# Kernel tuning notes

Hardware: AMD Instinct MI355X
Metric: run time of the kernel (lower is better)

Reference implementation:

```python
import jax, jax.numpy as jnp
import numpy as np

N, D, E, DFF = 8192, 1024, 8, 4096


def setup_inputs() -> dict:
    key = jax.random.key(0)
    k1, k2, k3, k4 = jax.random.split(key, 4)
    x = jax.random.normal(k1, (N, D), dtype=jnp.float32)
    gate_w = jax.random.normal(k2, (D, E), dtype=jnp.float32) * 0.02
    w1 = jax.random.normal(k3, (E, D, DFF), dtype=jnp.float32) * 0.02
    w2 = jax.random.normal(k4, (E, DFF, D), dtype=jnp.float32) * 0.02
    return {"x": x, "gate_w": gate_w, "w1": w1, "w2": w2, "top_k": 2}


def reference(x, gate_w, w1, w2, top_k):
    # Router: softmax over experts, top-k, renormalize top-k weights.
    gate_logits = x @ gate_w                          # [N, E]
    gate_probs = jax.nn.softmax(gate_logits, axis=-1)  # [N, E]
    top_w, top_i = jax.lax.top_k(gate_probs, top_k)    # [N, k]
    top_w = top_w / jnp.sum(top_w, axis=-1, keepdims=True)
    # Dense combine weights: zero except at the top-k experts per token.
    n = x.shape[0]
    dense_w = jnp.zeros_like(gate_probs).at[jnp.arange(n)[:, None], top_i].set(top_w)  # [N, E]
    # Per-expert SiLU MLP, weighted combine. Loop over small fixed E.
    y = jnp.zeros_like(x)
    for e in range(w1.shape[0]):
        h = jax.nn.silu(x @ w1[e]) @ w2[e]            # [N, D]
        y = y + dense_w[:, e:e + 1] * h
    return y
```

## Files before the change

### kernel.cpp

```cpp
#include <hip/hip_runtime.h>


#define N_TOK 8192
#define DIM   1024
#define NE    8
#define DFF   4096
#define BM 128
#define BN 128
#define BK 64
#define QE 4
#define KS2 2
#define NT2 (DFF / KS2 / BK)

typedef unsigned short u16;
typedef short bf16x8 __attribute__((ext_vector_type(8)));
typedef float f32x4  __attribute__((ext_vector_type(4)));

#define TOKE_OFF   0u
#define TOKW_OFF   32768u
#define TLIST_OFF  65536u
#define WLIST_OFF  131072u
#define COUNTS_OFF 196608u
#define BASEP_OFF  196672u
#define CURSOR_OFF 196736u
#define XB_OFF     1048576u
#define H_OFF      17825792u
#define WT_OFF     152043520u

__device__ __forceinline__ float bf2f(u16 h) {
    return __uint_as_float(((unsigned)h) << 16);
}
__device__ __forceinline__ u16 f2bf(float f) {
    unsigned u = __float_as_uint(f);
    unsigned r = u + 0x7FFFu + ((u >> 16) & 1u);
    return (u16)(r >> 16);
}

#define GLL16(g, l)                                                             \
    __builtin_amdgcn_global_load_lds(                                           \
        (const __attribute__((address_space(1))) unsigned int*)(g),             \
        (__attribute__((address_space(3))) unsigned int*)(l), 16, 0, 0)

__global__ __launch_bounds__(256) void convtrans(
        const float* __restrict__ in, u16* __restrict__ out, int R, int C) {
    __shared__ float t[32][33];
    int z = blockIdx.z;
    const float* src = in  + (size_t)z * R * C;
    u16*         dst = out + (size_t)z * R * C;
    int c0 = blockIdx.x * 32, r0 = blockIdx.y * 32;
    int tx = threadIdx.x & 7, ty = threadIdx.x >> 3;
    float4 v = *(const float4*)&src[(size_t)(r0 + ty) * C + c0 + tx * 4];
    t[tx * 4 + 0][ty] = v.x;  t[tx * 4 + 1][ty] = v.y;
    t[tx * 4 + 2][ty] = v.z;  t[tx * 4 + 3][ty] = v.w;
    __syncthreads();
    ushort4 o;
    o.x = f2bf(t[ty][tx * 4 + 0]);  o.y = f2bf(t[ty][tx * 4 + 1]);
    o.z = f2bf(t[ty][tx * 4 + 2]);  o.w = f2bf(t[ty][tx * 4 + 3]);
    *(ushort4*)&dst[(size_t)(c0 + ty) * R + r0 + tx * 4] = o;
}

__global__ __launch_bounds__(256) void gate_kernel(
        const float* __restrict__ x, const float* __restrict__ gw,
        u16* __restrict__ xb, int* __restrict__ tok_e, float* __restrict__ tok_w,
        int* __restrict__ counts) {
    __shared__ float gsm[NE * DIM];
    __shared__ int hcnt[NE];
    int tid = threadIdx.x;
    if (tid < NE) hcnt[tid] = 0;
    for (int i = tid; i < NE * DIM; i += 256) {
        int d = i >> 3, e = i & 7;
        gsm[e * DIM + d] = gw[i];
    }
    __syncthreads();
    int lane = tid & 63, wid = tid >> 6;
    int t0 = blockIdx.x * 32 + wid * 8;
    for (int tt = 0; tt < 8; ++tt) {
        int t = t0 + tt;
        const float4* xr  = (const float4*)(x  + (size_t)t * DIM);
        ushort4*      xbr = (ushort4*)(xb + (size_t)t * DIM);
        float acc[NE];
#pragma unroll
        for (int e = 0; e < NE; ++e) acc[e] = 0.f;
#pragma unroll
        for (int j = 0; j < 4; ++j) {
            float4 xv = xr[j * 64 + lane];
            ushort4 o;
            o.x = f2bf(xv.x); o.y = f2bf(xv.y); o.z = f2bf(xv.z); o.w = f2bf(xv.w);
            xbr[j * 64 + lane] = o;
            int dbase = (j * 64 + lane) * 4;
#pragma unroll
            for (int e = 0; e < NE; ++e) {
                float4 g = *(const float4*)&gsm[e * DIM + dbase];
                acc[e] += xv.x * g.x + xv.y * g.y + xv.z * g.z + xv.w * g.w;
            }
        }
#pragma unroll
        for (int off = 32; off > 0; off >>= 1) {
#pragma unroll
            for (int e = 0; e < NE; ++e) acc[e] += __shfl_xor(acc[e], off, 64);
        }
        if (lane == 0) {
            int a = 0;
#pragma unroll
            for (int e = 1; e < NE; ++e) if (acc[e] > acc[a]) a = e;
            int b = (a == 0) ? 1 : 0;
#pragma unroll
            for (int e = 0; e < NE; ++e) if (e != a && acc[e] > acc[b]) b = e;
            float wa = 1.f / (1.f + __expf(acc[b] - acc[a]));
            tok_e[t] = (a << 3) | b;
            tok_w[t] = wa;
            atomicAdd(&hcnt[a], 1);
            atomicAdd(&hcnt[b], 1);
        }
    }
    __syncthreads();
    if (tid < NE) atomicAdd(&counts[tid], hcnt[tid]);
}

__global__ void scan_kernel(const int* __restrict__ counts, int* __restrict__ basep,
                            int* __restrict__ cursor) {
    if (threadIdx.x == 0) {
        int s = 0;
        for (int e = 0; e < NE; ++e) { basep[e] = s; s += counts[e]; cursor[e] = 0; }
    }
}

__global__ void assign_kernel(const int* __restrict__ tok_e, const float* __restrict__ tok_w,
                              const int* __restrict__ basep, int* __restrict__ cursor,
                              int* __restrict__ tlist, float* __restrict__ wlist) {
    int t = blockIdx.x * 256 + threadIdx.x;
    if (t >= N_TOK) return;
    int ee = tok_e[t];
    int a = ee >> 3, b = ee & 7;
    float wa = tok_w[t];
    int pa = atomicAdd(&cursor[a], 1);
    int sa = basep[a] + pa;
    tlist[sa] = t;  wlist[sa] = wa;
    int pb = atomicAdd(&cursor[b], 1);
    int sb = basep[b] + pb;
    tlist[sb] = t;  wlist[sb] = 1.f - wa;
}

__global__ __launch_bounds__(256) void gemm1_silu(
        const u16* __restrict__ xb, const u16* __restrict__ w1t,
        const int* __restrict__ tlist, const int* __restrict__ counts,
        const int* __restrict__ basep, u16* __restrict__ H, int ebase) {
    int bx = blockIdx.x;
    int le = bx >> 11;
    int e  = ebase + le;
    int mt = (bx >> 5) & 63;
    int nt = bx & 31;
    int cnt = counts[e];
    int row0 = mt * BM;
    if (row0 >= cnt) return;
    int nv = cnt - row0; if (nv > BM) nv = BM;
    int gb = basep[e] + row0;

    __shared__ __align__(16) u16 As[BM * BK];
    __shared__ __align__(16) u16 Bs[BN * BK];

    int tid = threadIdx.x;
    int lane = tid & 63, wid = tid >> 6;
    int wm = (wid & 1) * 64, wn = (wid >> 1) * 64;

    const u16* ga[4]; const u16* gbp[4]; int loff[4];
#pragma unroll
    for (int i = 0; i < 4; ++i) {
        int cidx = (wid * 4 + i) * 64 + lane;
        int row = cidx >> 3;
        int cg  = (cidx & 7) ^ (row & 7);
        int ra  = (row < nv) ? row : 0;
        ga[i]  = xb + (size_t)tlist[gb + ra] * DIM + cg * 8;
        gbp[i] = w1t + ((size_t)le * DFF + (size_t)nt * BN + row) * DIM + cg * 8;
        loff[i] = (wid * 4 + i) * 512;
    }

    f32x4 acc[4][4];
#pragma unroll
    for (int i = 0; i < 4; ++i)
#pragma unroll
        for (int j = 0; j < 4; ++j) acc[i][j] = (f32x4){0.f, 0.f, 0.f, 0.f};

    for (int k0 = 0; k0 < DIM; k0 += BK) {
#pragma unroll
        for (int i = 0; i < 4; ++i) {
            GLL16(ga[i] + k0, &As[loff[i]]);
            GLL16(gbp[i] + k0, &Bs[loff[i]]);
        }
        __syncthreads();
#pragma unroll
        for (int ks = 0; ks < 2; ++ks) {
            int kc = ks * 4 + (lane >> 4);
            bf16x8 af[4], bfr[4];
#pragma unroll
            for (int mi = 0; mi < 4; ++mi) {
                int r = wm + mi * 16 + (lane & 15);
                af[mi] = *(const bf16x8*)&As[(r * 8 + (kc ^ (r & 7))) * 8];
            }
#pragma unroll
            for (int ni = 0; ni < 4; ++ni) {
                int r = wn + ni * 16 + (lane & 15);
                bfr[ni] = *(const bf16x8*)&Bs[(r * 8 + (kc ^ (r & 7))) * 8];
            }
#pragma unroll
            for (int mi = 0; mi < 4; ++mi)
#pragma unroll
                for (int ni = 0; ni < 4; ++ni)
                    acc[mi][ni] = __builtin_amdgcn_mfma_f32_16x16x32_bf16(
                        af[mi], bfr[ni], acc[mi][ni], 0, 0, 0);
        }
        __syncthreads();
    }
#pragma unroll
    for (int mi = 0; mi < 4; ++mi) {
#pragma unroll
        for (int r = 0; r < 4; ++r) {
            int row = wm + mi * 16 + (lane >> 4) * 4 + r;
            if (row < nv) {
                size_t ho = (size_t)(gb + row) * DFF + nt * BN + wn + (lane & 15);
#pragma unroll
                for (int ni = 0; ni < 4; ++ni) {
                    float v = acc[mi][ni][r];
                    H[ho + ni * 16] = f2bf(v / (1.f + __expf(-v)));
                }
            }
        }
    }
}

__global__ __launch_bounds__(256) void gemm2_combine(
        const u16* __restrict__ H, const u16* __restrict__ w2t,
        const int* __restrict__ tlist, const float* __restrict__ wlist,
        const int* __restrict__ counts, const int* __restrict__ basep,
        float* __restrict__ y, int ebase) {
    int bx = blockIdx.x;
    int le  = bx >> 10;
    int mt  = (bx >> 4) & 63;
    int nt  = (bx >> 1) & 7;
    int ksp = bx & 1;
    int e   = ebase + le;
    int cnt = counts[e];
    int row0 = mt * BM;
    if (row0 >= cnt) return;
    int nv = cnt - row0; if (nv > BM) nv = BM;
    int gb = basep[e] + row0;

    __shared__ __align__(16) u16 As[2][BM * BK];
    __shared__ __align__(16) u16 Bs[2][BN * BK];

    int tid = threadIdx.x;
    int lane = tid & 63, wid = tid >> 6;
    int wm = (wid & 1) * 64, wn = (wid >> 1) * 64;

    const u16* ga[4]; const u16* gbp[4]; int loff[4];
#pragma unroll
    for (int i = 0; i < 4; ++i) {
        int cidx = (wid * 4 + i) * 64 + lane;
        int row = cidx >> 3;
        int cg  = (cidx & 7) ^ (row & 7);
        int ra  = (row < nv) ? row : 0;
        ga[i]  = H + (size_t)(gb + ra) * DFF + cg * 8;
        gbp[i] = w2t + ((size_t)le * DIM + (size_t)nt * BN + row) * DFF + cg * 8;
        loff[i] = (wid * 4 + i) * 512;
    }

    f32x4 acc[4][4];
#pragma unroll
    for (int i = 0; i < 4; ++i)
#pragma unroll
        for (int j = 0; j < 4; ++j) acc[i][j] = (f32x4){0.f, 0.f, 0.f, 0.f};

#define STAGE2(buf, kk)                                                         \
    do {                                                                        \
        _Pragma("unroll")                                                       \
        for (int i = 0; i < 4; ++i) {                                           \
            GLL16(ga[i] + (kk), &As[buf][loff[i]]);                             \
            GLL16(gbp[i] + (kk), &Bs[buf][loff[i]]);                            \
        }                                                                       \
    } while (0)

#define COMPUTE2(buf)                                                           \
    do {                                                                        \
        _Pragma("unroll")                                                       \
        for (int ks = 0; ks < 2; ++ks) {                                        \
            int kc = ks * 4 + (lane >> 4);                                      \
            bf16x8 af[4], bfr[4];                                               \
            _Pragma("unroll")                                                   \
            for (int mi = 0; mi < 4; ++mi) {                                    \
                int r = wm + mi * 16 + (lane & 15);                             \
                af[mi] = *(const bf16x8*)&As[buf][(r * 8 + (kc ^ (r & 7))) * 8];\
            }                                                                   \
            _Pragma("unroll")                                                   \
            for (int ni = 0; ni < 4; ++ni) {                                    \
                int r = wn + ni * 16 + (lane & 15);                             \
                bfr[ni] = *(const bf16x8*)&Bs[buf][(r * 8 + (kc ^ (r & 7))) * 8];\
            }                                                                   \
            _Pragma("unroll")                                                   \
            for (int mi = 0; mi < 4; ++mi)                                      \
                _Pragma("unroll")                                               \
                for (int ni = 0; ni < 4; ++ni)                                  \
                    acc[mi][ni] = __builtin_amdgcn_mfma_f32_16x16x32_bf16(      \
                        af[mi], bfr[ni], acc[mi][ni], 0, 0, 0);                 \
        }                                                                       \
    } while (0)

    int kbeg = ksp * (DFF / KS2);
    STAGE2(0, kbeg);
    int cur = 0;
    for (int t = 0; t < NT2 - 1; ++t) {
        STAGE2(cur ^ 1, kbeg + (t + 1) * BK);
        asm volatile("s_waitcnt vmcnt(8)" ::: "memory");
        __builtin_amdgcn_s_barrier();
        __builtin_amdgcn_sched_barrier(0);
        COMPUTE2(cur);
        __builtin_amdgcn_s_barrier();
        cur ^= 1;
    }
    asm volatile("s_waitcnt vmcnt(0)" ::: "memory");
    __builtin_amdgcn_s_barrier();
    __builtin_amdgcn_sched_barrier(0);
    COMPUTE2(cur);

#pragma unroll
    for (int mi = 0; mi < 4; ++mi) {
#pragma unroll
        for (int r = 0; r < 4; ++r) {
            int row = wm + mi * 16 + (lane >> 4) * 4 + r;
            if (row < nv) {
                int gslot = gb + row;
                int t = tlist[gslot];
                float w = wlist[gslot];
                size_t yo = (size_t)t * DIM + nt * BN + wn + (lane & 15);
#pragma unroll
                for (int ni = 0; ni < 4; ++ni)
                    atomicAdd(&y[yo + ni * 16], w * acc[mi][ni][r]);
            }
        }
    }
#undef STAGE2
#undef COMPUTE2
}

extern "C" void kernel_launch(void* const* d_in, const int* in_sizes, int n_in,
                              void* d_out, int out_size, void* d_ws, size_t ws_size,
                              hipStream_t stream) {
    const float* x  = (const float*)d_in[0];
    const float* gw = (const float*)d_in[1];
    const float* w1 = (const float*)d_in[2];
    const float* w2 = (const float*)d_in[3];
    float* y = (float*)d_out;

    char* ws = (char*)d_ws;
    int*   tok_e  = (int*)(ws + TOKE_OFF);
    float* tok_w  = (float*)(ws + TOKW_OFF);
    int*   tlist  = (int*)(ws + TLIST_OFF);
    float* wlist  = (float*)(ws + WLIST_OFF);
    int*   counts = (int*)(ws + COUNTS_OFF);
    int*   basep  = (int*)(ws + BASEP_OFF);
    int*   cursor = (int*)(ws + CURSOR_OFF);
    u16*   xb     = (u16*)(ws + XB_OFF);
    u16*   H      = (u16*)(ws + H_OFF);
    u16*   wt     = (u16*)(ws + WT_OFF);

    hipMemsetAsync(counts, 0, 32, stream);
    hipMemsetAsync(y, 0, (size_t)N_TOK * DIM * sizeof(float), stream);
    gate_kernel<<<N_TOK / 32, 256, 0, stream>>>(x, gw, xb, tok_e, tok_w, counts);
    scan_kernel<<<1, 64, 0, stream>>>(counts, basep, cursor);
    assign_kernel<<<N_TOK / 256, 256, 0, stream>>>(tok_e, tok_w, basep, cursor, tlist, wlist);
    for (int q = 0; q < NE / QE; ++q) {
        convtrans<<<dim3(DFF / 32, DIM / 32, QE), 256, 0, stream>>>(
            w1 + (size_t)q * QE * DIM * DFF, wt, DIM, DFF);
        gemm1_silu<<<QE * 64 * 32, 256, 0, stream>>>(xb, wt, tlist, counts, basep, H, q * QE);
    }
    for (int q = 0; q < NE / QE; ++q) {
        convtrans<<<dim3(DIM / 32, DFF / 32, QE), 256, 0, stream>>>(
            w2 + (size_t)q * QE * DFF * DIM, wt, DFF, DIM);
        gemm2_combine<<<QE * 64 * 8 * KS2, 256, 0, stream>>>(H, wt, tlist, wlist, counts,
                                                             basep, y, q * QE);
    }
}
```

Measured before the change: 952.8 us.

## Use 256x256 tiles, compact work tables, and double-buffered gemm1

Both expert GEMMs move to 256x256 tiles with 512-thread blocks (8 waves, 128x64 per wave), which raises operand reuse per LDS load. The scan kernel now builds a compact per-group table of (expert, row-block) entries, so blocks index real work instead of exiting early on empty tiles. Block indices are also swizzled so neighbouring blocks share A/B tiles. gemm1 gains the same double-buffered global-to-LDS pipeline gemm2 already had. The costs are more LDS and more accumulator registers per block, which lowers occupancy, and grid sizes are hardcoded to fit a bounded number of tiles.

```diff
diff --git a/kernel.cpp b/kernel.cpp
--- a/kernel.cpp
+++ b/kernel.cpp
@@ -5,12 +5,13 @@
 #define DIM   1024
 #define NE    8
 #define DFF   4096
-#define BM 128
-#define BN 128
+#define BM 256
+#define BN 256
 #define BK 64
 #define QE 4
 #define KS2 2
-#define NT2 (DFF / KS2 / BK)
+#define NIT1 (DIM / BK)
+#define NIT2 (DFF / KS2 / BK)
 
 typedef unsigned short u16;
 typedef short bf16x8 __attribute__((ext_vector_type(8)));
@@ -23,6 +24,7 @@
 #define COUNTS_OFF 196608u
 #define BASEP_OFF  196672u
 #define CURSOR_OFF 196736u
+#define QTAB_OFF   197120u
 #define XB_OFF     1048576u
 #define H_OFF      17825792u
 #define WT_OFF     152043520u
@@ -118,10 +120,22 @@
 }
 
 __global__ void scan_kernel(const int* __restrict__ counts, int* __restrict__ basep,
-                            int* __restrict__ cursor) {
+                            int* __restrict__ cursor, int* __restrict__ qtab) {
     if (threadIdx.x == 0) {
         int s = 0;
         for (int e = 0; e < NE; ++e) { basep[e] = s; s += counts[e]; cursor[e] = 0; }
+        for (int q = 0; q < 2; ++q) {
+            int n = 0;
+            for (int le = 0; le < QE; ++le) {
+                int e = q * QE + le;
+                int c = counts[e];
+                for (int r0 = 0; r0 < c; r0 += BM) {
+                    qtab[q * 80 + 1 + n] = (e << 20) | r0;
+                    ++n;
+                }
+            }
+            qtab[q * 80] = n;
+        }
     }
 }
 
@@ -141,78 +155,100 @@
     tlist[sb] = t;  wlist[sb] = 1.f - wa;
 }
 
-__global__ __launch_bounds__(256) void gemm1_silu(
+__global__ __launch_bounds__(512, 2) void gemm1_silu(
         const u16* __restrict__ xb, const u16* __restrict__ w1t,
         const int* __restrict__ tlist, const int* __restrict__ counts,
-        const int* __restrict__ basep, u16* __restrict__ H, int ebase) {
+        const int* __restrict__ basep, const int* __restrict__ qtab,
+        u16* __restrict__ H, int ebase) {
     int bx = blockIdx.x;
-    int le = bx >> 11;
-    int e  = ebase + le;
-    int mt = (bx >> 5) & 63;
-    int nt = bx & 31;
+    int work = (bx & ~127) | ((bx & 7) << 4) | ((bx & 127) >> 3);
+    int g = work >> 4, nt = work & 15;
+    const int* tab = qtab + (ebase >> 2) * 80;
+    if (g >= tab[0]) return;
+    int pk = tab[1 + g];
+    int e = pk >> 20, row0 = pk & 0xFFFFF;
+    int le = e - ebase;
     int cnt = counts[e];
-    int row0 = mt * BM;
-    if (row0 >= cnt) return;
     int nv = cnt - row0; if (nv > BM) nv = BM;
     int gb = basep[e] + row0;
 
-    __shared__ __align__(16) u16 As[BM * BK];
-    __shared__ __align__(16) u16 Bs[BN * BK];
+    __shared__ __align__(16) u16 As[2][BM * BK];
+    __shared__ __align__(16) u16 Bs[2][BN * BK];
 
     int tid = threadIdx.x;
     int lane = tid & 63, wid = tid >> 6;
-    int wm = (wid & 1) * 64, wn = (wid >> 1) * 64;
+    int wm = (wid & 1) * 128, wn = (wid >> 1) * 64;
 
     const u16* ga[4]; const u16* gbp[4]; int loff[4];
 #pragma unroll
     for (int i = 0; i < 4; ++i) {
-        int cidx = (wid * 4 + i) * 64 + lane;
+        int cidx = wid * 256 + i * 64 + lane;
         int row = cidx >> 3;
         int cg  = (cidx & 7) ^ (row & 7);
         int ra  = (row < nv) ? row : 0;
         ga[i]  = xb + (size_t)tlist[gb + ra] * DIM + cg * 8;
         gbp[i] = w1t + ((size_t)le * DFF + (size_t)nt * BN + row) * DIM + cg * 8;
-        loff[i] = (wid * 4 + i) * 512;
-    }
-
-    f32x4 acc[4][4];
-#pragma unroll
-    for (int i = 0; i < 4; ++i)
+        loff[i] = wid * 2048 + i * 512;
+    }
+
+    f32x4 acc[8][4];
+#pragma unroll
+    for (int i = 0; i < 8; ++i)
 #pragma unroll
         for (int j = 0; j < 4; ++j) acc[i][j] = (f32x4){0.f, 0.f, 0.f, 0.f};
 
-    for (int k0 = 0; k0 < DIM; k0 += BK) {
-#pragma unroll
-        for (int i = 0; i < 4; ++i) {
-            GLL16(ga[i] + k0, &As[loff[i]]);
-            GLL16(gbp[i] + k0, &Bs[loff[i]]);
-        }
-        __syncthreads();
-#pragma unroll
-        for (int ks = 0; ks < 2; ++ks) {
-            int kc = ks * 4 + (lane >> 4);
-            bf16x8 af[4], bfr[4];
-#pragma unroll
-            for (int mi = 0; mi < 4; ++mi) {
-                int r = wm + mi * 16 + (lane & 15);
-                af[mi] = *(const bf16x8*)&As[(r * 8 + (kc ^ (r & 7))) * 8];
-            }
-#pragma unroll
-            for (int ni = 0; ni < 4; ++ni) {
-                int r = wn + ni * 16 + (lane & 15);
-                bfr[ni] = *(const bf16x8*)&Bs[(r * 8 + (kc ^ (r & 7))) * 8];
-            }
-#pragma unroll
-            for (int mi = 0; mi < 4; ++mi)
-#pragma unroll
-                for (int ni = 0; ni < 4; ++ni)
-                    acc[mi][ni] = __builtin_amdgcn_mfma_f32_16x16x32_bf16(
-                        af[mi], bfr[ni], acc[mi][ni], 0, 0, 0);
-        }
-        __syncthreads();
-    }
-#pragma unroll
-    for (int mi = 0; mi < 4; ++mi) {
+#define STAGE1(buf, kk)                                                         \
+    do {                                                                        \
+        _Pragma("unroll")                                                       \
+        for (int i = 0; i < 4; ++i) {                                           \
+            GLL16(ga[i] + (kk), &As[buf][loff[i]]);                             \
+            GLL16(gbp[i] + (kk), &Bs[buf][loff[i]]);                            \
+        }                                                                       \
+    } while (0)
+
+#define COMPUTE1(buf)                                                           \
+    do {                                                                        \
+        _Pragma("unroll")                                                       \
+        for (int ks = 0; ks < 2; ++ks) {                                        \
+            int kc = ks * 4 + (lane >> 4);                                      \
+            bf16x8 af[8], bfr[4];                                               \
+            _Pragma("unroll")                                                   \
+            for (int mi = 0; mi < 8; ++mi) {                                    \
+                int r = wm + mi * 16 + (lane & 15);                             \
+                af[mi] = *(const bf16x8*)&As[buf][(r * 8 + (kc ^ (r & 7))) * 8];\
+            }                                                                   \
+            _Pragma("unroll")                                                   \
+            for (int ni = 0; ni < 4; ++ni) {                                    \
+                int r = wn + ni * 16 + (lane & 15);                             \
+                bfr[ni] = *(const bf16x8*)&Bs[buf][(r * 8 + (kc ^ (r & 7))) * 8];\
+            }                                                                   \
+            _Pragma("unroll")                                                   \
+            for (int mi = 0; mi < 8; ++mi)                                      \
+                _Pragma("unroll")                                               \
+                for (int ni = 0; ni < 4; ++ni)                                  \
+                    acc[mi][ni] = __builtin_amdgcn_mfma_f32_16x16x32_bf16(      \
+                        af[mi], bfr[ni], acc[mi][ni], 0, 0, 0);                 \
+        }                                                                       \
+    } while (0)
+
+    STAGE1(0, 0);
+    int cur = 0;
+    for (int t = 0; t < NIT1 - 1; ++t) {
+        STAGE1(cur ^ 1, (t + 1) * BK);
+        asm volatile("s_waitcnt vmcnt(8)" ::: "memory");
+        __builtin_amdgcn_s_barrier();
+        __builtin_amdgcn_sched_barrier(0);
+        COMPUTE1(cur);
+        __builtin_amdgcn_s_barrier();
+        cur ^= 1;
+    }
+    asm volatile("s_waitcnt vmcnt(0)" ::: "memory");
+    __builtin_amdgcn_s_barrier();
+    __builtin_amdgcn_sched_barrier(0);
+    COMPUTE1(cur);
+
+#pragma unroll
+    for (int mi = 0; mi < 8; ++mi) {
 #pragma unroll
         for (int r = 0; r < 4; ++r) {
             int row = wm + mi * 16 + (lane >> 4) * 4 + r;
@@ -226,22 +262,24 @@
             }
         }
     }
-}
-
-__global__ __launch_bounds__(256) void gemm2_combine(
+#undef STAGE1
+#undef COMPUTE1
+}
+
+__global__ __launch_bounds__(512, 2) void gemm2_combine(
         const u16* __restrict__ H, const u16* __restrict__ w2t,
         const int* __restrict__ tlist, const float* __restrict__ wlist,
         const int* __restrict__ counts, const int* __restrict__ basep,
-        float* __restrict__ y, int ebase) {
+        const int* __restrict__ qtab, float* __restrict__ y, int ebase) {
     int bx = blockIdx.x;
-    int le  = bx >> 10;
-    int mt  = (bx >> 4) & 63;
-    int nt  = (bx >> 1) & 7;
-    int ksp = bx & 1;
-    int e   = ebase + le;
+    int work = (bx & ~63) | ((bx & 7) << 3) | ((bx & 63) >> 3);
+    int g = work >> 3, nt = (work >> 1) & 3, ksp = work & 1;
+    const int* tab = qtab + (ebase >> 2) * 80;
+    if (g >= tab[0]) return;
+    int pk = tab[1 + g];
+    int e = pk >> 20, row0 = pk & 0xFFFFF;
+    int le = e - ebase;
     int cnt = counts[e];
-    int row0 = mt * BM;
-    if (row0 >= cnt) return;
     int nv = cnt - row0; if (nv > BM) nv = BM;
     int gb = basep[e] + row0;
 
@@ -250,23 +288,23 @@
 
     int tid = threadIdx.x;
     int lane = tid & 63, wid = tid >> 6;
-    int wm = (wid & 1) * 64, wn = (wid >> 1) * 64;
+    int wm = (wid & 1) * 128, wn = (wid >> 1) * 64;
 
     const u16* ga[4]; const u16* gbp[4]; int loff[4];
 #pragma unroll
     for (int i = 0; i < 4; ++i) {
-        int cidx = (wid * 4 + i) * 64 + lane;
+        int cidx = wid * 256 + i * 64 + lane;
         int row = cidx >> 3;
         int cg  = (cidx & 7) ^ (row & 7);
         int ra  = (row < nv) ? row : 0;
         ga[i]  = H + (size_t)(gb + ra) * DFF + cg * 8;
         gbp[i] = w2t + ((size_t)le * DIM + (size_t)nt * BN + row) * DFF + cg * 8;
-        loff[i] = (wid * 4 + i) * 512;
-    }
-
-    f32x4 acc[4][4];
-#pragma unroll
-    for (int i = 0; i < 4; ++i)
+        loff[i] = wid * 2048 + i * 512;
+    }
+
+    f32x4 acc[8][4];
+#pragma unroll
+    for (int i = 0; i < 8; ++i)
 #pragma unroll
         for (int j = 0; j < 4; ++j) acc[i][j] = (f32x4){0.f, 0.f, 0.f, 0.f};
 
@@ -284,9 +322,9 @@
         _Pragma("unroll")                                                       \
         for (int ks = 0; ks < 2; ++ks) {                                        \
             int kc = ks * 4 + (lane >> 4);                                      \
-            bf16x8 af[4], bfr[4];                                               \
-            _Pragma("unroll")                                                   \
-            for (int mi = 0; mi < 4; ++mi) {                                    \
+            bf16x8 af[8], bfr[4];                                               \
+            _Pragma("unroll")                                                   \
+            for (int mi = 0; mi < 8; ++mi) {                                    \
                 int r = wm + mi * 16 + (lane & 15);                             \
                 af[mi] = *(const bf16x8*)&As[buf][(r * 8 + (kc ^ (r & 7))) * 8];\
             }                                                                   \
@@ -296,7 +334,7 @@
                 bfr[ni] = *(const bf16x8*)&Bs[buf][(r * 8 + (kc ^ (r & 7))) * 8];\
             }                                                                   \
             _Pragma("unroll")                                                   \
-            for (int mi = 0; mi < 4; ++mi)                                      \
+            for (int mi = 0; mi < 8; ++mi)                                      \
                 _Pragma("unroll")                                               \
                 for (int ni = 0; ni < 4; ++ni)                                  \
                     acc[mi][ni] = __builtin_amdgcn_mfma_f32_16x16x32_bf16(      \
@@ -307,7 +345,7 @@
     int kbeg = ksp * (DFF / KS2);
     STAGE2(0, kbeg);
     int cur = 0;
-    for (int t = 0; t < NT2 - 1; ++t) {
+    for (int t = 0; t < NIT2 - 1; ++t) {
         STAGE2(cur ^ 1, kbeg + (t + 1) * BK);
         asm volatile("s_waitcnt vmcnt(8)" ::: "memory");
         __builtin_amdgcn_s_barrier();
@@ -322,7 +360,7 @@
     COMPUTE2(cur);
 
 #pragma unroll
-    for (int mi = 0; mi < 4; ++mi) {
+    for (int mi = 0; mi < 8; ++mi) {
 #pragma unroll
         for (int r = 0; r < 4; ++r) {
             int row = wm + mi * 16 + (lane >> 4) * 4 + r;
@@ -358,6 +396,7 @@
     int*   counts = (int*)(ws + COUNTS_OFF);
     int*   basep  = (int*)(ws + BASEP_OFF);
     int*   cursor = (int*)(ws + CURSOR_OFF);
+    int*   qtab   = (int*)(ws + QTAB_OFF);
     u16*   xb     = (u16*)(ws + XB_OFF);
     u16*   H      = (u16*)(ws + H_OFF);
     u16*   wt     = (u16*)(ws + WT_OFF);
@@ -365,17 +404,17 @@
     hipMemsetAsync(counts, 0, 32, stream);
     hipMemsetAsync(y, 0, (size_t)N_TOK * DIM * sizeof(float), stream);
     gate_kernel<<<N_TOK / 32, 256, 0, stream>>>(x, gw, xb, tok_e, tok_w, counts);
-    scan_kernel<<<1, 64, 0, stream>>>(counts, basep, cursor);
+    scan_kernel<<<1, 64, 0, stream>>>(counts, basep, cursor, qtab);
     assign_kernel<<<N_TOK / 256, 256, 0, stream>>>(tok_e, tok_w, basep, cursor, tlist, wlist);
     for (int q = 0; q < NE / QE; ++q) {
         convtrans<<<dim3(DFF / 32, DIM / 32, QE), 256, 0, stream>>>(
             w1 + (size_t)q * QE * DIM * DFF, wt, DIM, DFF);
-        gemm1_silu<<<QE * 64 * 32, 256, 0, stream>>>(xb, wt, tlist, counts, basep, H, q * QE);
+        gemm1_silu<<<1152, 512, 0, stream>>>(xb, wt, tlist, counts, basep, qtab, H, q * QE);
     }
     for (int q = 0; q < NE / QE; ++q) {
         convtrans<<<dim3(DIM / 32, DFF / 32, QE), 256, 0, stream>>>(
             w2 + (size_t)q * QE * DFF * DIM, wt, DFF, DIM);
-        gemm2_combine<<<QE * 64 * 8 * KS2, 256, 0, stream>>>(H, wt, tlist, wlist, counts,
-                                                             basep, y, q * QE);
-    }
-}
+        gemm2_combine<<<576, 512, 0, stream>>>(H, wt, tlist, wlist, counts, basep, qtab,
+                                               y, q * QE);
+    }
+}
```

After: 1.009 ms. 1.06x slower.

## Compact tile schedule via work table, XCD swizzle, register-staged GEMM2 pipeline

Applied to the files above, without the earlier changes.

The scan kernel now builds a compact table of (expert, row-tile) work items, so the GEMM grids launch only populated tiles instead of early-exiting empty ones. Block IDs are remapped with an 8-way swizzle so adjacent tiles land on the same XCD, and all experts are processed in one group when the workspace is large enough. GEMM2 replaces direct global-to-LDS loads with register-staged double buffering and requests two blocks per CU. The fixed 136-tile grid bound relies on the counts, and the register staging raises register pressure.

```diff
diff --git a/kernel.cpp b/kernel.cpp
--- a/kernel.cpp
+++ b/kernel.cpp
@@ -8,9 +8,10 @@
 #define BM 128
 #define BN 128
 #define BK 64
-#define QE 4
 #define KS2 2
 #define NT2 (DFF / KS2 / BK)
+#define NT1 (DIM / BK)
+#define QSTR 160
 
 typedef unsigned short u16;
 typedef short bf16x8 __attribute__((ext_vector_type(8)));
@@ -23,13 +24,12 @@
 #define COUNTS_OFF 196608u
 #define BASEP_OFF  196672u
 #define CURSOR_OFF 196736u
+#define QTAB_OFF   197120u
 #define XB_OFF     1048576u
 #define H_OFF      17825792u
 #define WT_OFF     152043520u
-
-__device__ __forceinline__ float bf2f(u16 h) {
-    return __uint_as_float(((unsigned)h) << 16);
-}
+#define WS_MERGED  219152384ull
+
 __device__ __forceinline__ u16 f2bf(float f) {
     unsigned u = __float_as_uint(f);
     unsigned r = u + 0x7FFFu + ((u >> 16) & 1u);
@@ -118,10 +118,20 @@
 }
 
 __global__ void scan_kernel(const int* __restrict__ counts, int* __restrict__ basep,
-                            int* __restrict__ cursor) {
+                            int* __restrict__ cursor, int* __restrict__ qtab, int eper) {
     if (threadIdx.x == 0) {
         int s = 0;
         for (int e = 0; e < NE; ++e) { basep[e] = s; s += counts[e]; cursor[e] = 0; }
+        int ngrp = NE / eper;
+        for (int qq = 0; qq < ngrp; ++qq) {
+            int n = 0;
+            for (int le = 0; le < eper; ++le) {
+                int e = qq * eper + le;
+                int c = counts[e];
+                for (int r0 = 0; r0 < c; r0 += BM) { qtab[qq * QSTR + 1 + n] = (e << 20) | r0; ++n; }
+            }
+            qtab[qq * QSTR] = n;
+        }
     }
 }
 
@@ -141,18 +151,26 @@
     tlist[sb] = t;  wlist[sb] = 1.f - wa;
 }
 
+__device__ __forceinline__ int swz_lid(int bx, int na) {
+    if (bx >= na) return bx;
+    int x = bx & 7, idx = bx >> 3, q = na >> 3, r2 = na & 7;
+    return (x < r2 ? x * (q + 1) : r2 * (q + 1) + (x - r2) * q) + idx;
+}
+
 __global__ __launch_bounds__(256) void gemm1_silu(
         const u16* __restrict__ xb, const u16* __restrict__ w1t,
         const int* __restrict__ tlist, const int* __restrict__ counts,
-        const int* __restrict__ basep, u16* __restrict__ H, int ebase) {
-    int bx = blockIdx.x;
-    int le = bx >> 11;
-    int e  = ebase + le;
-    int mt = (bx >> 5) & 63;
-    int nt = bx & 31;
+        const int* __restrict__ basep, const int* __restrict__ qtab,
+        u16* __restrict__ H, int ebase, int tabsel) {
+    const int* tab = qtab + tabsel * QSTR;
+    int na = tab[0] * 32;
+    int lid = swz_lid(blockIdx.x, na);
+    int g = lid >> 5, nt = lid & 31;
+    if (g >= tab[0]) return;
+    int pk = tab[1 + g];
+    int e = pk >> 20, row0 = pk & 0xFFFFF;
+    int le = e - ebase;
     int cnt = counts[e];
-    int row0 = mt * BM;
-    if (row0 >= cnt) return;
     int nv = cnt - row0; if (nv > BM) nv = BM;
     int gb = basep[e] + row0;
 
@@ -228,22 +246,23 @@
     }
 }
 
-__global__ __launch_bounds__(256) void gemm2_combine(
+__global__ __launch_bounds__(256, 2) void gemm2_combine(
         const u16* __restrict__ H, const u16* __restrict__ w2t,
         const int* __restrict__ tlist, const float* __restrict__ wlist,
         const int* __restrict__ counts, const int* __restrict__ basep,
-        float* __restrict__ y, int ebase) {
-    int bx = blockIdx.x;
-    int le  = bx >> 10;
-    int mt  = (bx >> 4) & 63;
-    int nt  = (bx >> 1) & 7;
-    int ksp = bx & 1;
-    int e   = ebase + le;
+        const int* __restrict__ qtab, float* __restrict__ y, int ebase, int tabsel) {
+    const int* tab = qtab + tabsel * QSTR;
+    int na = tab[0] * 8 * KS2;
+    int lid = swz_lid(blockIdx.x, na);
+    int g = lid >> 4, nt = (lid >> 1) & 7, ksp = lid & 1;
+    if (g >= tab[0]) return;
+    int pk = tab[1 + g];
+    int e = pk >> 20, row0 = pk & 0xFFFFF;
+    int le = e - ebase;
     int cnt = counts[e];
-    int row0 = mt * BM;
-    if (row0 >= cnt) return;
     int nv = cnt - row0; if (nv > BM) nv = BM;
     int gb = basep[e] + row0;
+    int kbase = ksp * (DFF / KS2);
 
     __shared__ __align__(16) u16 As[2][BM * BK];
     __shared__ __align__(16) u16 Bs[2][BN * BK];
@@ -252,16 +271,15 @@
     int lane = tid & 63, wid = tid >> 6;
     int wm = (wid & 1) * 64, wn = (wid >> 1) * 64;
 
-    const u16* ga[4]; const u16* gbp[4]; int loff[4];
+    const u16* gA[4]; const u16* gB[4]; int woff[4];
 #pragma unroll
     for (int i = 0; i < 4; ++i) {
-        int cidx = (wid * 4 + i) * 64 + lane;
-        int row = cidx >> 3;
-        int cg  = (cidx & 7) ^ (row & 7);
-        int ra  = (row < nv) ? row : 0;
-        ga[i]  = H + (size_t)(gb + ra) * DFF + cg * 8;
-        gbp[i] = w2t + ((size_t)le * DIM + (size_t)nt * BN + row) * DFF + cg * 8;
-        loff[i] = (wid * 4 + i) * 512;
+        int c = i * 256 + tid;
+        int row = c >> 3, j = c & 7;
+        int ra = (row < nv) ? row : 0;
+        gA[i] = H + (size_t)(gb + ra) * DFF + kbase + j * 8;
+        gB[i] = w2t + ((size_t)le * DIM + (size_t)nt * BN + row) * DFF + kbase + j * 8;
+        woff[i] = (row * 8 + (j ^ (row & 7))) * 8;
     }
 
     f32x4 acc[4][4];
@@ -270,12 +288,23 @@
 #pragma unroll
         for (int j = 0; j < 4; ++j) acc[i][j] = (f32x4){0.f, 0.f, 0.f, 0.f};
 
-#define STAGE2(buf, kk)                                                         \
+    bf16x8 sA0[4], sB0[4], sA1[4], sB1[4];
+
+#define LOADSET(sa, sb, kk)                                                     \
     do {                                                                        \
         _Pragma("unroll")                                                       \
         for (int i = 0; i < 4; ++i) {                                           \
-            GLL16(ga[i] + (kk), &As[buf][loff[i]]);                             \
-            GLL16(gbp[i] + (kk), &Bs[buf][loff[i]]);                            \
+            sa[i] = *(const bf16x8*)(gA[i] + (kk));                             \
+            sb[i] = *(const bf16x8*)(gB[i] + (kk));                             \
+        }                                                                       \
+    } while (0)
+
+#define WRITESET(sa, sb, buf)                                                   \
+    do {                                                                        \
+        _Pragma("unroll")                                                       \
+        for (int i = 0; i < 4; ++i) {                                           \
+            *(bf16x8*)&As[buf][woff[i]] = sa[i];                                \
+            *(bf16x8*)&Bs[buf][woff[i]] = sb[i];                                \
         }                                                                       \
     } while (0)
 
@@ -304,22 +333,37 @@
         }                                                                       \
     } while (0)
 
-    int kbeg = ksp * (DFF / KS2);
-    STAGE2(0, kbeg);
-    int cur = 0;
-    for (int t = 0; t < NT2 - 1; ++t) {
-        STAGE2(cur ^ 1, kbeg + (t + 1) * BK);
-        asm volatile("s_waitcnt vmcnt(8)" ::: "memory");
-        __builtin_amdgcn_s_barrier();
-        __builtin_amdgcn_sched_barrier(0);
-        COMPUTE2(cur);
-        __builtin_amdgcn_s_barrier();
-        cur ^= 1;
-    }
-    asm volatile("s_waitcnt vmcnt(0)" ::: "memory");
-    __builtin_amdgcn_s_barrier();
-    __builtin_amdgcn_sched_barrier(0);
-    COMPUTE2(cur);
+#define LGKM0_BAR()                                                             \
+    do {                                                                        \
+        asm volatile("s_waitcnt lgkmcnt(0)" ::: "memory");                      \
+        __builtin_amdgcn_s_barrier();                                           \
+    } while (0)
+
+    LOADSET(sA0, sB0, 0);
+    LOADSET(sA1, sB1, BK);
+    WRITESET(sA0, sB0, 0);
+    LOADSET(sA0, sB0, 2 * BK);
+    LGKM0_BAR();
+
+    for (int t = 0; t < NT2; t += 2) {
+        COMPUTE2(0);
+        if (t + 1 < NT2) {
+            WRITESET(sA1, sB1, 1);
+            if (t + 3 < NT2) LOADSET(sA1, sB1, (t + 3) * BK);
+        }
+        LGKM0_BAR();
+        if (t + 1 >= NT2) break;
+        COMPUTE2(1);
+        if (t + 2 < NT2) {
+            WRITESET(sA0, sB0, 0);
+            if (t + 4 < NT2) LOADSET(sA0, sB0, (t + 4) * BK);
+        }
+        LGKM0_BAR();
+    }
+#undef LOADSET
+#undef WRITESET
+#undef COMPUTE2
+#undef LGKM0_BAR
 
 #pragma unroll
     for (int mi = 0; mi < 4; ++mi) {
@@ -337,8 +381,6 @@
             }
         }
     }
-#undef STAGE2
-#undef COMPUTE2
 }
 
 extern "C" void kernel_launch(void* const* d_in, const int* in_sizes, int n_in,
@@ -358,24 +400,29 @@
     int*   counts = (int*)(ws + COUNTS_OFF);
     int*   basep  = (int*)(ws + BASEP_OFF);
     int*   cursor = (int*)(ws + CURSOR_OFF);
+    int*   qtab   = (int*)(ws + QTAB_OFF);
     u16*   xb     = (u16*)(ws + XB_OFF);
     u16*   H      = (u16*)(ws + H_OFF);
     u16*   wt     = (u16*)(ws + WT_OFF);
 
+    int nq = (ws_size >= WS_MERGED) ? 1 : 2;
+    int eper = NE / nq;
+
     hipMemsetAsync(counts, 0, 32, stream);
     hipMemsetAsync(y, 0, (size_t)N_TOK * DIM * sizeof(float), stream);
     gate_kernel<<<N_TOK / 32, 256, 0, stream>>>(x, gw, xb, tok_e, tok_w, counts);
-    scan_kernel<<<1, 64, 0, stream>>>(counts, basep, cursor);
+    scan_kernel<<<1, 64, 0, stream>>>(counts, basep, cursor, qtab, eper);
     assign_kernel<<<N_TOK / 256, 256, 0, stream>>>(tok_e, tok_w, basep, cursor, tlist, wlist);
-    for (int q = 0; q < NE / QE; ++q) {
-        convtrans<<<dim3(DFF / 32, DIM / 32, QE), 256, 0, stream>>>(
-            w1 + (size_t)q * QE * DIM * DFF, wt, DIM, DFF);
-        gemm1_silu<<<QE * 64 * 32, 256, 0, stream>>>(xb, wt, tlist, counts, basep, H, q * QE);
-    }
-    for (int q = 0; q < NE / QE; ++q) {
-        convtrans<<<dim3(DIM / 32, DFF / 32, QE), 256, 0, stream>>>(
-            w2 + (size_t)q * QE * DFF * DIM, wt, DFF, DIM);
-        gemm2_combine<<<QE * 64 * 8 * KS2, 256, 0, stream>>>(H, wt, tlist, wlist, counts,
-                                                             basep, y, q * QE);
-    }
-}
+    for (int q = 0; q < nq; ++q) {
+        convtrans<<<dim3(DFF / 32, DIM / 32, eper), 256, 0, stream>>>(
+            w1 + (size_t)q * eper * DIM * DFF, wt, DIM, DFF);
+        gemm1_silu<<<136 * 32, 256, 0, stream>>>(xb, wt, tlist, counts, basep, qtab,
+                                                 H, q * eper, q);
+    }
+    for (int q = 0; q < nq; ++q) {
+        convtrans<<<dim3(DIM / 32, DFF / 32, eper), 256, 0, stream>>>(
+            w2 + (size_t)q * eper * DFF * DIM, wt, DFF, DIM);
+        gemm2_combine<<<136 * 8 * KS2, 256, 0, stream>>>(H, wt, tlist, wlist, counts,
+                                                         basep, qtab, y, q * eper, q);
+    }
+}
```

Result: faster. 853.3 us (-10.4%).
